# Performance work log

Measured on AMD Instinct MI355X. Metric: run time of the kernel, lower is better.

Reference implementation:

```python
import jax, jax.numpy as jnp
import numpy as np

IN_FEATURES = 4096
OUT_FEATURES = 4096  # % 16 == 0, so pad_out = 0
BATCH, SEQ = 4, 2048


def setup_inputs() -> dict:
    key = jax.random.key(0)
    k_x, k_w, k_b = jax.random.split(key, 3)
    # int8 activations and weights (W8A8)
    x = jax.random.randint(k_x, (BATCH, SEQ, IN_FEATURES), -128, 128, dtype=jnp.int32).astype(jnp.int8)
    # weight stored as (in_features, out_features), matching qlinear.weight layout
    weight = jax.random.randint(k_w, (IN_FEATURES, OUT_FEATURES), -128, 128, dtype=jnp.int32).astype(jnp.int8)
    # a: scalar input scale; b: per-output-channel dequant/requant scale
    a = jnp.full((1, 1), 0.0123, dtype=jnp.float32)
    b = jax.random.uniform(k_b, (1, OUT_FEATURES), dtype=jnp.float32, minval=0.001, maxval=0.02)
    return {"x": x, "weight": weight, "a": a, "b": b}


def reference(x, weight, a, b):
    # x: [B, S, K] int8; weight: [K, N] int8; a: [1,1] f32; b: [1,N] f32
    x_shape = x.shape
    x2d = x.reshape(-1, x_shape[-1])
    acc = jnp.matmul(x2d, weight, preferred_element_type=jnp.int32)
    # fused dequant (scalar a) + per-channel requant (b), round-to-nearest, saturate to int8
    y_f = acc.astype(jnp.float32) * a * b  # [T, N]
    y = jnp.clip(jnp.round(y_f), -128.0, 127.0).astype(jnp.int8)
    return y.reshape(*x_shape[:-1], -1)
```

## Files before the change

### kernel.cpp

```cpp
#include <hip/hip_runtime.h>
#include <stdint.h>

#define M_DIM 8192
#define N_DIM 4096
#define K_DIM 4096
#define BM 128
#define BN 128
#define BK 64

typedef int v4i __attribute__((ext_vector_type(4)));
typedef unsigned u32;

__device__ __forceinline__ void gll16(const void* g, void* l) {
  __builtin_amdgcn_global_load_lds(
      (const __attribute__((address_space(1))) void*)g,
      (__attribute__((address_space(3))) void*)l, 16, 0, 0);
}

__device__ __forceinline__ u32 pack4(const int4 v) {
  return (v.x & 0xffu) | ((v.y & 0xffu) << 8) | ((v.z & 0xffu) << 16) |
         ((u32)(v.w & 0xffu) << 24);
}

__global__ __launch_bounds__(256) void detect_i32(const int* __restrict__ X,
                                                  u32* __restrict__ flag) {
  __shared__ int ok;
  if (threadIdx.x == 0) ok = 1;
  __syncthreads();
  int good = 1;
  for (int i = threadIdx.x; i < 1024; i += 256) {
    const int w = X[i];
    good &= (w == (int)(int8_t)(w & 0xff));
  }
  if (!good) atomicAnd(&ok, 0);
  __syncthreads();
  if (threadIdx.x == 0) *flag = (u32)ok;
}

__global__ __launch_bounds__(256) void pack_x_ad(const void* __restrict__ Xin,
                                                 u32* __restrict__ out,
                                                 const u32* __restrict__ flag) {
  const bool i32 = (*flag != 0);
  const int base = blockIdx.x * 1024 + threadIdx.x;
  if (i32) {
    const int4* in = (const int4*)Xin;
#pragma unroll
    for (int j = 0; j < 4; ++j) {
      const int idx = base + j * 256;
      out[idx] = pack4(in[idx]);
    }
  } else {
    const u32* in = (const u32*)Xin;
#pragma unroll
    for (int j = 0; j < 4; ++j) {
      const int idx = base + j * 256;
      out[idx] = in[idx];
    }
  }
}

__global__ __launch_bounds__(256) void packT_w_ad(const void* __restrict__ Wv,
                                                  int8_t* __restrict__ WT,
                                                  const u32* __restrict__ flag) {
  __shared__ u32 lds[64 * 21];
  const bool i32 = (*flag != 0);
  const int tid = threadIdx.x;
  const int tk = blockIdx.x & 63;
  const int tn = blockIdx.x >> 6;
  const int k0 = tk * 64, n0 = tn * 64;

#pragma unroll
  for (int j = 0; j < 4; ++j) {
    const int id = j * 256 + tid;
    const int k = id >> 4, c = id & 15;
    u32 word;
    if (i32) {
      const int4 v =
          *(const int4*)((const int*)Wv + (size_t)(k0 + k) * N_DIM + n0 + c * 4);
      word = pack4(v);
    } else {
      word = *(const u32*)((const int8_t*)Wv + (size_t)(k0 + k) * N_DIM + n0 +
                           c * 4);
    }
    lds[k * 21 + c] = word;
  }
  __syncthreads();
  const int kd = tid & 15, nq = tid >> 4;
  const u32 d0 = lds[(kd * 4 + 0) * 21 + nq];
  const u32 d1 = lds[(kd * 4 + 1) * 21 + nq];
  const u32 d2 = lds[(kd * 4 + 2) * 21 + nq];
  const u32 d3 = lds[(kd * 4 + 3) * 21 + nq];
  u32* outp = (u32*)WT;
#pragma unroll
  for (int i = 0; i < 4; ++i) {
    const u32 e = ((d0 >> (8 * i)) & 0xffu) | (((d1 >> (8 * i)) & 0xffu) << 8) |
                  (((d2 >> (8 * i)) & 0xffu) << 16) |
                  (((d3 >> (8 * i)) & 0xffu) << 24);
    const int n = n0 + nq * 4 + i;
    outp[(size_t)n * (K_DIM / 4) + (k0 / 4) + kd] = e;
  }
}

__device__ __forceinline__ void epilogue(const v4i acc[4][4], float a,
                                         const float* __restrict__ bScale,
                                         int* __restrict__ Y, int bm, int bn,
                                         int wm, int wn, int quad, int l16) {
  const int nBase = bn * BN + wn * 64 + l16;
  float bs[4];
#pragma unroll
  for (int ni = 0; ni < 4; ++ni) bs[ni] = bScale[nBase + ni * 16];
#pragma unroll
  for (int mi = 0; mi < 4; ++mi) {
    const int m0 = bm * BM + wm * 64 + mi * 16 + quad * 4;
#pragma unroll
    for (int r = 0; r < 4; ++r) {
      int* row = Y + (size_t)(m0 + r) * N_DIM + nBase;
#pragma unroll
      for (int ni = 0; ni < 4; ++ni) {
        float v = ((float)acc[mi][ni][r] * a) * bs[ni];
        v = rintf(v);
        v = fminf(fmaxf(v, -128.f), 127.f);
        row[ni * 16] = (int)v;
      }
    }
  }
}

__global__ __launch_bounds__(256) void gemm_packed(
    const int8_t* __restrict__ X, const int8_t* __restrict__ WT,
    const float* __restrict__ aScale, const float* __restrict__ bScale,
    int* __restrict__ Y) {
  __shared__ __align__(16) int8_t As[BM * BK];
  __shared__ __align__(16) int8_t Bs[BN * BK];
  const int tid = threadIdx.x;
  const int lane = tid & 63, wave = tid >> 6;
  const int quad = lane >> 4, l16 = lane & 15;
  const int wm = wave & 1, wn = wave >> 1;
  const int bn = blockIdx.x & 31;
  const int bm = blockIdx.x >> 5;

  const int r0 = tid >> 2;
  const int c0 = (tid & 3) * 16;
  const int8_t* Ag0 = X + (size_t)(bm * BM + r0) * K_DIM + c0;
  const int8_t* Ag1 = Ag0 + (size_t)64 * K_DIM;
  const int8_t* Bg0 = WT + (size_t)(bn * BN + r0) * K_DIM + c0;
  const int8_t* Bg1 = Bg0 + (size_t)64 * K_DIM;
  int8_t* Al0 = As + tid * 16;
  int8_t* Al1 = Al0 + 4096;
  int8_t* Bl0 = Bs + tid * 16;
  int8_t* Bl1 = Bl0 + 4096;

  v4i acc[4][4] = {};
  const int8_t* aLds = As + (wm * 64 + l16) * BK + quad * 16;
  const int8_t* bLds = Bs + (wn * 64 + l16) * BK + quad * 16;

  for (int k0 = 0; k0 < K_DIM; k0 += BK) {
    gll16(Ag0 + k0, Al0);
    gll16(Ag1 + k0, Al1);
    gll16(Bg0 + k0, Bl0);
    gll16(Bg1 + k0, Bl1);
    __syncthreads();
    v4i af[4], bf[4];
#pragma unroll
    for (int i = 0; i < 4; ++i) af[i] = *(const v4i*)(aLds + i * 16 * BK);
#pragma unroll
    for (int i = 0; i < 4; ++i) bf[i] = *(const v4i*)(bLds + i * 16 * BK);
#pragma unroll
    for (int mi = 0; mi < 4; ++mi)
#pragma unroll
      for (int ni = 0; ni < 4; ++ni)
        acc[mi][ni] = __builtin_amdgcn_mfma_i32_16x16x64_i8(
            af[mi], bf[ni], acc[mi][ni], 0, 0, 0);
    __syncthreads();
  }
  epilogue(acc, aScale[0], bScale, Y, bm, bn, wm, wn, quad, l16);
}

__global__ __launch_bounds__(256) void gemm_inA(
    const void* __restrict__ Xv, const int8_t* __restrict__ WT,
    const float* __restrict__ aScale, const float* __restrict__ bScale,
    int* __restrict__ Y, const u32* __restrict__ flag) {
  __shared__ __align__(16) int8_t As[BM * BK];
  __shared__ __align__(16) int8_t Bs[BN * BK];
  const bool i32 = (*flag != 0);
  const int tid = threadIdx.x;
  const int lane = tid & 63, wave = tid >> 6;
  const int quad = lane >> 4, l16 = lane & 15;
  const int wm = wave & 1, wn = wave >> 1;
  const int bn = blockIdx.x & 31;
  const int bm = blockIdx.x >> 5;

  const int r0 = tid >> 2;
  const int c0 = (tid & 3) * 16;
  const int8_t* Bg0 = WT + (size_t)(bn * BN + r0) * K_DIM + c0;
  const int8_t* Bg1 = Bg0 + (size_t)64 * K_DIM;
  int8_t* Al0 = As + tid * 16;
  int8_t* Al1 = Al0 + 4096;
  int8_t* Bl0 = Bs + tid * 16;
  int8_t* Bl1 = Bl0 + 4096;

  v4i acc[4][4] = {};
  const int8_t* aLds = As + (wm * 64 + l16) * BK + quad * 16;
  const int8_t* bLds = Bs + (wn * 64 + l16) * BK + quad * 16;

  if (i32) {
    const int* Xg0 = (const int*)Xv + (size_t)(bm * BM + r0) * K_DIM + c0;
    const int* Xg1 = Xg0 + (size_t)64 * K_DIM;
    for (int k0 = 0; k0 < K_DIM; k0 += BK) {
      gll16(Bg0 + k0, Bl0);
      gll16(Bg1 + k0, Bl1);
      const int4* p0 = (const int4*)(Xg0 + k0);
      const int4* p1 = (const int4*)(Xg1 + k0);
      uint4 w0, w1;
      w0.x = pack4(p0[0]); w0.y = pack4(p0[1]);
      w0.z = pack4(p0[2]); w0.w = pack4(p0[3]);
      w1.x = pack4(p1[0]); w1.y = pack4(p1[1]);
      w1.z = pack4(p1[2]); w1.w = pack4(p1[3]);
      *(uint4*)Al0 = w0;
      *(uint4*)Al1 = w1;
      __syncthreads();
      v4i af[4], bf[4];
#pragma unroll
      for (int i = 0; i < 4; ++i) af[i] = *(const v4i*)(aLds + i * 16 * BK);
#pragma unroll
      for (int i = 0; i < 4; ++i) bf[i] = *(const v4i*)(bLds + i * 16 * BK);
#pragma unroll
      for (int mi = 0; mi < 4; ++mi)
#pragma unroll
        for (int ni = 0; ni < 4; ++ni)
          acc[mi][ni] = __builtin_amdgcn_mfma_i32_16x16x64_i8(
              af[mi], bf[ni], acc[mi][ni], 0, 0, 0);
      __syncthreads();
    }
  } else {
    const int8_t* Ag0 = (const int8_t*)Xv + (size_t)(bm * BM + r0) * K_DIM + c0;
    const int8_t* Ag1 = Ag0 + (size_t)64 * K_DIM;
    for (int k0 = 0; k0 < K_DIM; k0 += BK) {
      gll16(Ag0 + k0, Al0);
      gll16(Ag1 + k0, Al1);
      gll16(Bg0 + k0, Bl0);
      gll16(Bg1 + k0, Bl1);
      __syncthreads();
      v4i af[4], bf[4];
#pragma unroll
      for (int i = 0; i < 4; ++i) af[i] = *(const v4i*)(aLds + i * 16 * BK);
#pragma unroll
      for (int i = 0; i < 4; ++i) bf[i] = *(const v4i*)(bLds + i * 16 * BK);
#pragma unroll
      for (int mi = 0; mi < 4; ++mi)
#pragma unroll
        for (int ni = 0; ni < 4; ++ni)
          acc[mi][ni] = __builtin_amdgcn_mfma_i32_16x16x64_i8(
              af[mi], bf[ni], acc[mi][ni], 0, 0, 0);
      __syncthreads();
    }
  }
  epilogue(acc, aScale[0], bScale, Y, bm, bn, wm, wn, quad, l16);
}

extern "C" void kernel_launch(void* const* d_in, const int* in_sizes, int n_in,
                              void* d_out, int out_size, void* d_ws,
                              size_t ws_size, hipStream_t stream) {
  const void* Xv = d_in[0];
  const void* Wv = d_in[1];
  const float* a = (const float*)d_in[2];
  const float* b = (const float*)d_in[3];
  int* Y = (int*)d_out;

  const size_t xB = (size_t)M_DIM * K_DIM;
  const size_t wB = (size_t)N_DIM * K_DIM;
  const int grid = (M_DIM / BM) * (N_DIM / BN);

  if (ws_size >= xB + wB + 64) {
    int8_t* Xp = (int8_t*)d_ws;
    int8_t* WT = (int8_t*)d_ws + xB;
    u32* flag = (u32*)((int8_t*)d_ws + xB + wB);
    detect_i32<<<1, 256, 0, stream>>>((const int*)Xv, flag);
    pack_x_ad<<<(M_DIM * K_DIM / 4) / 1024, 256, 0, stream>>>(Xv, (u32*)Xp,
                                                              flag);
    packT_w_ad<<<(K_DIM / 64) * (N_DIM / 64), 256, 0, stream>>>(Wv, WT, flag);
    gemm_packed<<<grid, 256, 0, stream>>>(Xp, WT, a, b, Y);
  } else if (ws_size >= wB + 64) {
    int8_t* WT = (int8_t*)d_ws;
    u32* flag = (u32*)((int8_t*)d_ws + wB);
    detect_i32<<<1, 256, 0, stream>>>((const int*)Xv, flag);
    packT_w_ad<<<(K_DIM / 64) * (N_DIM / 64), 256, 0, stream>>>(Wv, WT, flag);
    gemm_inA<<<grid, 256, 0, stream>>>(Xv, WT, a, b, Y, flag);
  } else {
    int8_t* WT = (int8_t*)d_ws;
    u32* flag = (u32*)((int8_t*)d_ws + (ws_size >= wB + 4 ? wB : 0));
    detect_i32<<<1, 256, 0, stream>>>((const int*)Xv, flag);
    packT_w_ad<<<(K_DIM / 64) * (N_DIM / 64), 256, 0, stream>>>(Wv, WT, flag);
    gemm_inA<<<grid, 256, 0, stream>>>(Xv, WT, a, b, Y, flag);
  }
}
```

Before: 425.8 us.

## Replace packed GEMM with 256x256-tile, 4-stage LDS-pipelined 512-thread kernel

```diff
diff --git a/kernel.cpp b/kernel.cpp
--- a/kernel.cpp
+++ b/kernel.cpp
@@ -126,54 +126,118 @@
   }
 }
 
-__global__ __launch_bounds__(256) void gemm_packed(
+__global__ __launch_bounds__(512, 2) void gemm_256(
     const int8_t* __restrict__ X, const int8_t* __restrict__ WT,
     const float* __restrict__ aScale, const float* __restrict__ bScale,
     int* __restrict__ Y) {
-  __shared__ __align__(16) int8_t As[BM * BK];
-  __shared__ __align__(16) int8_t Bs[BN * BK];
+  __shared__ __align__(16) int8_t lds[131072];
   const int tid = threadIdx.x;
-  const int lane = tid & 63, wave = tid >> 6;
+  const int lane = tid & 63;
+  const int wave = tid >> 6;
   const int quad = lane >> 4, l16 = lane & 15;
-  const int wm = wave & 1, wn = wave >> 1;
-  const int bn = blockIdx.x & 31;
-  const int bm = blockIdx.x >> 5;
-
-  const int r0 = tid >> 2;
-  const int c0 = (tid & 3) * 16;
-  const int8_t* Ag0 = X + (size_t)(bm * BM + r0) * K_DIM + c0;
-  const int8_t* Ag1 = Ag0 + (size_t)64 * K_DIM;
-  const int8_t* Bg0 = WT + (size_t)(bn * BN + r0) * K_DIM + c0;
-  const int8_t* Bg1 = Bg0 + (size_t)64 * K_DIM;
-  int8_t* Al0 = As + tid * 16;
-  int8_t* Al1 = Al0 + 4096;
-  int8_t* Bl0 = Bs + tid * 16;
-  int8_t* Bl1 = Bl0 + 4096;
-
-  v4i acc[4][4] = {};
-  const int8_t* aLds = As + (wm * 64 + l16) * BK + quad * 16;
-  const int8_t* bLds = Bs + (wn * 64 + l16) * BK + quad * 16;
-
-  for (int k0 = 0; k0 < K_DIM; k0 += BK) {
-    gll16(Ag0 + k0, Al0);
-    gll16(Ag1 + k0, Al1);
-    gll16(Bg0 + k0, Bl0);
-    gll16(Bg1 + k0, Bl1);
-    __syncthreads();
+  const int wm = wave >> 2, wn = wave & 3;
+
+  const int swz = (blockIdx.x & 7) * 64 + (blockIdx.x >> 3);
+  const int bn = swz & 15, bm = swz >> 4;
+
+  const int clog = (((tid & 3) ^ ((tid >> 3) & 3)) << 4);
+  const int pc = quad ^ ((l16 >> 1) & 3);
+
+  const int8_t* xa = X + (size_t)(bm * 256 + (tid >> 2)) * K_DIM + clog;
+  const int8_t* xb = WT + (size_t)(bn * 256 + (tid >> 2)) * K_DIM + clog;
+  int8_t* ldsA = lds + tid * 16;
+  int8_t* ldsB = lds + 65536 + tid * 16;
+  const int8_t* aBase = lds + (wm * 128 + l16) * 64 + pc * 16;
+  const int8_t* bBase = lds + 65536 + (wn * 64 + l16) * 64 + pc * 16;
+
+  v4i acc[8][4] = {};
+
+  gll16(xa, ldsA);
+  gll16(xa + (size_t)128 * K_DIM, ldsA + 8192);
+  gll16(xb, ldsB);
+  gll16(xb + (size_t)128 * K_DIM, ldsB + 8192);
+  gll16(xa + 64, ldsA + 16384);
+  gll16(xa + (size_t)128 * K_DIM + 64, ldsA + 16384 + 8192);
+  gll16(xb + 64, ldsB + 16384);
+  gll16(xb + (size_t)128 * K_DIM + 64, ldsB + 16384 + 8192);
+  asm volatile("s_waitcnt vmcnt(4)" ::: "memory");
+  __builtin_amdgcn_s_barrier();
+
+  for (int g = 0; g < 64; ++g) {
+    const int soff = (g & 3) << 14;
+    const int poff = ((g + 2) & 3) << 14;
+    const bool pre = (g + 2) < 64;
     v4i af[4], bf[4];
 #pragma unroll
-    for (int i = 0; i < 4; ++i) af[i] = *(const v4i*)(aLds + i * 16 * BK);
-#pragma unroll
-    for (int i = 0; i < 4; ++i) bf[i] = *(const v4i*)(bLds + i * 16 * BK);
+    for (int i = 0; i < 4; ++i)
+      af[i] = *(const v4i*)(aBase + soff + i * 1024);
+#pragma unroll
+    for (int i = 0; i < 4; ++i)
+      bf[i] = *(const v4i*)(bBase + soff + i * 1024);
+    if (pre) {
+      const int8_t* s = xa + (size_t)(g + 2) * 64;
+      gll16(s, ldsA + poff);
+      gll16(s + (size_t)128 * K_DIM, ldsA + poff + 8192);
+    }
+    __builtin_amdgcn_s_barrier();
+    asm volatile("s_waitcnt lgkmcnt(0)" ::: "memory");
+    __builtin_amdgcn_sched_barrier(0);
+    __builtin_amdgcn_s_setprio(1);
 #pragma unroll
     for (int mi = 0; mi < 4; ++mi)
 #pragma unroll
       for (int ni = 0; ni < 4; ++ni)
         acc[mi][ni] = __builtin_amdgcn_mfma_i32_16x16x64_i8(
             af[mi], bf[ni], acc[mi][ni], 0, 0, 0);
-    __syncthreads();
-  }
-  epilogue(acc, aScale[0], bScale, Y, bm, bn, wm, wn, quad, l16);
+    __builtin_amdgcn_s_setprio(0);
+    __builtin_amdgcn_s_barrier();
+
+#pragma unroll
+    for (int i = 0; i < 4; ++i)
+      af[i] = *(const v4i*)(aBase + soff + 4096 + i * 1024);
+    if (pre) {
+      const int8_t* s = xb + (size_t)(g + 2) * 64;
+      gll16(s, ldsB + poff);
+      gll16(s + (size_t)128 * K_DIM, ldsB + poff + 8192);
+    }
+    __builtin_amdgcn_s_barrier();
+    asm volatile("s_waitcnt lgkmcnt(0)" ::: "memory");
+    __builtin_amdgcn_sched_barrier(0);
+    __builtin_amdgcn_s_setprio(1);
+#pragma unroll
+    for (int mi = 0; mi < 4; ++mi)
+#pragma unroll
+      for (int ni = 0; ni < 4; ++ni)
+        acc[4 + mi][ni] = __builtin_amdgcn_mfma_i32_16x16x64_i8(
+            af[mi], bf[ni], acc[4 + mi][ni], 0, 0, 0);
+    __builtin_amdgcn_s_setprio(0);
+    if (g <= 61)
+      asm volatile("s_waitcnt vmcnt(4)" ::: "memory");
+    else
+      asm volatile("s_waitcnt vmcnt(0)" ::: "memory");
+    __builtin_amdgcn_s_barrier();
+  }
+
+  const float a = aScale[0];
+  const int nBase = bn * 256 + wn * 64 + l16;
+  float bs[4];
+#pragma unroll
+  for (int ni = 0; ni < 4; ++ni) bs[ni] = bScale[nBase + ni * 16];
+#pragma unroll
+  for (int mi = 0; mi < 8; ++mi) {
+    const int m0 = bm * 256 + wm * 128 + mi * 16 + quad * 4;
+#pragma unroll
+    for (int r = 0; r < 4; ++r) {
+      int* row = Y + (size_t)(m0 + r) * N_DIM + nBase;
+#pragma unroll
+      for (int ni = 0; ni < 4; ++ni) {
+        float v = ((float)acc[mi][ni][r] * a) * bs[ni];
+        v = rintf(v);
+        v = fminf(fmaxf(v, -128.f), 127.f);
+        row[ni * 16] = (int)v;
+      }
+    }
+  }
 }
 
 __global__ __launch_bounds__(256) void gemm_inA(
@@ -269,7 +333,6 @@
 
   const size_t xB = (size_t)M_DIM * K_DIM;
   const size_t wB = (size_t)N_DIM * K_DIM;
-  const int grid = (M_DIM / BM) * (N_DIM / BN);
 
   if (ws_size >= xB + wB + 64) {
     int8_t* Xp = (int8_t*)d_ws;
@@ -279,18 +342,21 @@
     pack_x_ad<<<(M_DIM * K_DIM / 4) / 1024, 256, 0, stream>>>(Xv, (u32*)Xp,
                                                               flag);
     packT_w_ad<<<(K_DIM / 64) * (N_DIM / 64), 256, 0, stream>>>(Wv, WT, flag);
-    gemm_packed<<<grid, 256, 0, stream>>>(Xp, WT, a, b, Y);
+    gemm_256<<<(M_DIM / 256) * (N_DIM / 256), 512, 0, stream>>>(Xp, WT, a, b,
+                                                                Y);
   } else if (ws_size >= wB + 64) {
     int8_t* WT = (int8_t*)d_ws;
     u32* flag = (u32*)((int8_t*)d_ws + wB);
     detect_i32<<<1, 256, 0, stream>>>((const int*)Xv, flag);
     packT_w_ad<<<(K_DIM / 64) * (N_DIM / 64), 256, 0, stream>>>(Wv, WT, flag);
-    gemm_inA<<<grid, 256, 0, stream>>>(Xv, WT, a, b, Y, flag);
+    gemm_inA<<<(M_DIM / BM) * (N_DIM / BN), 256, 0, stream>>>(Xv, WT, a, b, Y,
+                                                              flag);
   } else {
     int8_t* WT = (int8_t*)d_ws;
     u32* flag = (u32*)((int8_t*)d_ws + (ws_size >= wB + 4 ? wB : 0));
     detect_i32<<<1, 256, 0, stream>>>((const int*)Xv, flag);
     packT_w_ad<<<(K_DIM / 64) * (N_DIM / 64), 256, 0, stream>>>(Wv, WT, flag);
-    gemm_inA<<<grid, 256, 0, stream>>>(Xv, WT, a, b, Y, flag);
-  }
-}
+    gemm_inA<<<(M_DIM / BM) * (N_DIM / BN), 256, 0, stream>>>(Xv, WT, a, b, Y,
+                                                              flag);
+  }
+}
```

Result: faster. 408.0 us (-4.2%).
